# Kernel optimization log

Measured on AMD Instinct MI355X. Metric: run time of the kernel, lower is better.

The kernel has to match this reference:

```python
import jax, jax.numpy as jnp
import numpy as np

B, H, W, C = 16, 56, 56, 512
NUM_HEADS = 8
WS = 4  # window_size


def setup_inputs() -> dict:
    key = jax.random.key(0)
    k1, k2, k3, k4 = jax.random.split(key, 4)
    x = jax.random.normal(k1, (B, H, W, C), dtype=jnp.float32)
    w_qkv_h = jax.random.normal(k2, (3 * C, C), dtype=jnp.float32) * 0.02
    w_qkv_l = jax.random.normal(k3, (3 * C, C), dtype=jnp.float32) * 0.02
    w_proj = jax.random.normal(k4, (C, 2 * C), dtype=jnp.float32) * 0.02
    b_proj = jnp.zeros((C,), dtype=jnp.float32)
    return {"x": x, "w_qkv_h": w_qkv_h, "w_qkv_l": w_qkv_l,
            "w_proj": w_proj, "b_proj": b_proj}


def reference(x, w_qkv_h, w_qkv_l, w_proj, b_proj):
    b, h, w, c = x.shape
    nh = NUM_HEADS
    hd = c // nh
    nw = WS * WS  # tokens per window
    scale = c ** -0.5  # NOTE: original scales by full dim, not head dim

    # window partition: [B*H/ws*W/ws, ws*ws, C]
    xw = x.reshape(b, h // WS, WS, w // WS, WS, c)
    xw = xw.transpose(0, 1, 3, 2, 4, 5).reshape(-1, nw, c)

    # local branch qkv: [3, Nwin, nh, nw, hd]
    qkv_h = (xw @ w_qkv_h.T).reshape(-1, nw, 3, nh, hd).transpose(2, 0, 3, 1, 4)
    q_h, k_h, v_h = qkv_h[0], qkv_h[1], qkv_h[2]

    # global branch: average-pool each window to a single token [Nwin, 1, C]
    x_avg = x.reshape(b, h // WS, WS, w // WS, WS, c).mean(axis=(2, 4))
    x_avg = x_avg.reshape(-1, 1, c)
    qkv_l = (x_avg @ w_qkv_l.T).reshape(-1, 1, 3, nh, hd).transpose(2, 0, 3, 1, 4)
    q_l, k_l, v_l = qkv_l[0], qkv_l[1], qkv_l[2]

    # local window attention: [Nwin, nh, nw, nw]
    attn_h = jax.nn.softmax(jnp.einsum('bhqd,bhkd->bhqk', q_h, k_h) * scale, axis=-1)
    x_h = jnp.einsum('bhqk,bhkd->bhqd', attn_h, v_h)
    x_h = x_h.transpose(0, 2, 1, 3).reshape(-1, nw, c)

    # pooled global attention (1 token -> softmax over singleton = 1)
    attn_l = jax.nn.softmax(jnp.einsum('bhqd,bhkd->bhqk', q_l, k_l) * scale, axis=-1)
    x_l = jnp.einsum('bhqk,bhkd->bhqd', attn_l, v_l)
    x_l = x_l.transpose(0, 2, 1, 3).reshape(-1, 1, c)

    # concat local + broadcast global, project 2C -> C
    x_out = jnp.concatenate([x_h, jnp.broadcast_to(x_l, (x_l.shape[0], nw, c))], axis=-1)
    x_out = x_out @ w_proj.T + b_proj

    # window reverse
    x_out = x_out.reshape(b, h // WS, w // WS, WS, WS, c)
    x_out = x_out.transpose(0, 1, 3, 2, 4, 5).reshape(b, h, w, c)
    return x_out
```

## Files before the change

kernel.cpp:

```cpp
#include <hip/hip_runtime.h>


using bf16x8 = __attribute__((ext_vector_type(8))) short;
using f32x4  = __attribute__((ext_vector_type(4))) float;

#define SCALE 0.044194173824159216f

__device__ __forceinline__ unsigned short f2bf(float f) {
    union { float f; unsigned u; } v; v.f = f;
    unsigned u = v.u;
    return (unsigned short)((u + 0x7fffu + ((u >> 16) & 1u)) >> 16);
}

__device__ __forceinline__ void gl2lds16(const unsigned short* g, unsigned short* l) {
    __builtin_amdgcn_global_load_lds(
        (const __attribute__((address_space(1))) void*)g,
        (__attribute__((address_space(3))) void*)l, 16, 0, 0);
}

__global__ void k_prep_weights(const float* __restrict__ wqkv_h,
                               const float* __restrict__ wqkv_l,
                               const float* __restrict__ wproj,
                               unsigned short* __restrict__ WH,
                               unsigned short* __restrict__ WLV,
                               unsigned short* __restrict__ WP1,
                               unsigned short* __restrict__ WP2) {
    int i = blockIdx.x * 256 + threadIdx.x;
    if (i < 786432) {
        WH[i] = f2bf(wqkv_h[i]);
    } else {
        int j = i - 786432;
        int r = j >> 18;
        int t = j & 262143;
        int n = t >> 9, k = t & 511;
        if (r == 0)      WLV[t] = f2bf(wqkv_l[(1024 + n) * 512 + k]);
        else if (r == 1) WP1[t] = f2bf(wproj[n * 1024 + k]);
        else             WP2[t] = f2bf(wproj[n * 1024 + 512 + k]);
    }
}

__global__ void k_window_pool(const float* __restrict__ x,
                              unsigned short* __restrict__ XW,
                              unsigned short* __restrict__ XAVG) {
    int win = blockIdx.x * 2 + (threadIdx.x >> 7);
    int g = threadIdx.x & 127;
    int c = g * 4;
    int b = win / 196, rem = win % 196, wh = rem / 14, ww = rem % 14;
    float4 s = {0.f, 0.f, 0.f, 0.f};
    #pragma unroll
    for (int t = 0; t < 16; ++t) {
        int row = (b * 56 + wh * 4 + (t >> 2)) * 56 + ww * 4 + (t & 3);
        float4 v = *(const float4*)&x[(size_t)row * 512 + c];
        uint2 pk;
        pk.x = (unsigned)f2bf(v.x) | ((unsigned)f2bf(v.y) << 16);
        pk.y = (unsigned)f2bf(v.z) | ((unsigned)f2bf(v.w) << 16);
        *(uint2*)&XW[(size_t)(win * 16 + t) * 512 + c] = pk;
        s.x += v.x; s.y += v.y; s.z += v.z; s.w += v.w;
    }
    uint2 pa;
    pa.x = (unsigned)f2bf(s.x * 0.0625f) | ((unsigned)f2bf(s.y * 0.0625f) << 16);
    pa.y = (unsigned)f2bf(s.z * 0.0625f) | ((unsigned)f2bf(s.w * 0.0625f) << 16);
    *(uint2*)&XAVG[(size_t)win * 512 + c] = pa;
}

template <int NT>
__global__ void k_gemm512(const unsigned short* __restrict__ A,
                          const unsigned short* __restrict__ Bw,
                          unsigned short* __restrict__ outB,
                          float* __restrict__ outF,
                          const float* __restrict__ bias) {
    int wave = threadIdx.x >> 6, lane = threadIdx.x & 63;
    int quad = lane >> 4, l16 = lane & 15;
    int m0 = blockIdx.x * 64 + wave * 16;
    int n0 = blockIdx.y * (NT * 16);
    f32x4 acc[NT] = {};
    const unsigned short* arow = A + (size_t)(m0 + l16) * 512 + quad * 8;
    for (int kk = 0; kk < 16; ++kk) {
        bf16x8 a = *(const bf16x8*)(arow + kk * 32);
        #pragma unroll
        for (int nt = 0; nt < NT; ++nt) {
            bf16x8 b = *(const bf16x8*)(Bw + (size_t)(n0 + nt * 16 + l16) * 512 + kk * 32 + quad * 8);
            acc[nt] = __builtin_amdgcn_mfma_f32_16x16x32_bf16(a, b, acc[nt], 0, 0, 0);
        }
    }
    #pragma unroll
    for (int nt = 0; nt < NT; ++nt) {
        int col = n0 + nt * 16 + l16;
        float bv = (bias != nullptr) ? bias[col] : 0.f;
        #pragma unroll
        for (int r = 0; r < 4; ++r) {
            int row = m0 + quad * 4 + r;
            if (outF != nullptr) outF[(size_t)row * 512 + col] = acc[nt][r] + bv;
            else                 outB[(size_t)row * 512 + col] = f2bf(acc[nt][r]);
        }
    }
}

__global__ void __launch_bounds__(512, 4) k_fused(const unsigned short* __restrict__ XW,
                                                  const unsigned short* __restrict__ WH,
                                                  unsigned short* __restrict__ XH) {
    __shared__ __align__(16) char smem[81920];

    const int tid  = threadIdx.x;
    const int wave = tid >> 6, lane = tid & 63;
    const int quad = lane >> 4, l16 = lane & 15;
    const int mh = wave >> 2, nq = wave & 3;

    int id   = blockIdx.y * 392 + blockIdx.x;
    int s_   = id >> 3;
    int tb   = (id & 7) * 49 + (s_ >> 3);
    int head = s_ & 7;
    const int m0 = tb * 128;

    size_t aof[2];
    #pragma unroll
    for (int i = 0; i < 2; ++i) {
        int u = i * 512 + tid;
        int n = u >> 3;
        int gu = (u & 7) ^ (n & 7);
        aof[i] = (size_t)(m0 + n) * 512 + gu * 8;
    }
    size_t bof[3];
    #pragma unroll
    for (int i = 0; i < 3; ++i) {
        int u = i * 512 + tid;
        int n = u >> 3;
        int gu = (u & 7) ^ (n & 7);
        int nrow = (n >> 6) * 512 + head * 64 + (n & 63);
        bof[i] = (size_t)nrow * 512 + gu * 8;
    }

    unsigned short* const bufA[2] = { (unsigned short*)smem,
                                      (unsigned short*)(smem + 40960) };
    unsigned short* const bufB[2] = { (unsigned short*)(smem + 16384),
                                      (unsigned short*)(smem + 40960 + 16384) };

    f32x4 acc[4][3] = {};
    const int sx = l16 & 7;

    #pragma unroll
    for (int i = 0; i < 2; ++i)
        gl2lds16(XW + aof[i], bufA[0] + (i * 512 + wave * 64) * 8);
    #pragma unroll
    for (int i = 0; i < 3; ++i)
        gl2lds16(WH + bof[i], bufB[0] + (i * 512 + wave * 64) * 8);
    __syncthreads();

    #pragma unroll
    for (int ch = 0; ch < 8; ++ch) {
        unsigned short* As = bufA[ch & 1];
        unsigned short* Bs = bufB[ch & 1];
        if (ch < 7) {
            unsigned short* An = bufA[(ch + 1) & 1];
            unsigned short* Bn = bufB[(ch + 1) & 1];
            #pragma unroll
            for (int i = 0; i < 2; ++i)
                gl2lds16(XW + aof[i] + (ch + 1) * 64, An + (i * 512 + wave * 64) * 8);
            #pragma unroll
            for (int i = 0; i < 3; ++i)
                gl2lds16(WH + bof[i] + (ch + 1) * 64, Bn + (i * 512 + wave * 64) * 8);
        }
        #pragma unroll
        for (int kk = 0; kk < 2; ++kk) {
            int su = ((kk * 4 + quad) ^ sx) * 8;
            bf16x8 a[4], b[3];
            #pragma unroll
            for (int mf = 0; mf < 4; ++mf) {
                int row = mh * 64 + mf * 16 + l16;
                a[mf] = *(const bf16x8*)&As[row * 64 + (((kk * 4 + quad) ^ (row & 7)) ^ sx ^ (row & 7)) * 8];
            }
            #pragma unroll
            for (int j = 0; j < 3; ++j) {
                int brow = nq * 48 + j * 16 + l16;
                b[j] = *(const bf16x8*)&Bs[brow * 64 + (((kk * 4 + quad) ^ (brow & 7)) ^ sx ^ (brow & 7)) * 8];
            }
            #pragma unroll
            for (int mf = 0; mf < 4; ++mf)
                #pragma unroll
                for (int j = 0; j < 3; ++j)
                    acc[mf][j] = __builtin_amdgcn_mfma_f32_16x16x32_bf16(a[mf], b[j], acc[mf][j], 0, 0, 0);
        }
        __syncthreads();
    }

    {
        char* att = smem + mh * 33792;
        unsigned short* qs  = (unsigned short*)att;
        unsigned short* ks  = (unsigned short*)(att + 9216);
        unsigned short* vts = (unsigned short*)(att + 18432);
        #pragma unroll
        for (int j = 0; j < 3; ++j) {
            int cb = nq * 48 + j * 16;
            #pragma unroll
            for (int mf = 0; mf < 4; ++mf) {
                #pragma unroll
                for (int r = 0; r < 4; ++r) {
                    int tok = mf * 16 + quad * 4 + r;
                    unsigned short hv = f2bf(acc[mf][j][r]);
                    if (cb < 64)       qs[tok * 72 + cb + l16] = hv;
                    else if (cb < 128) ks[tok * 72 + (cb - 64) + l16] = hv;
                    else               vts[(cb - 128 + l16) * 88 + tok] = hv;
                }
            }
        }
    }
    __syncthreads();

    char* att = smem + (wave >> 2) * 33792;
    unsigned short* qs  = (unsigned short*)att;
    unsigned short* ks  = (unsigned short*)(att + 9216);
    unsigned short* vts = (unsigned short*)(att + 18432);
    unsigned short* Ps  = (unsigned short*)(att + 29696);
    const int lw = wave & 3, t0 = lw * 16;

    if (lw == 3) {
        #pragma unroll
        for (int i = 0; i < 16; ++i) vts[lane * 88 + 64 + i] = 0;
    }
    {
        int prow = lane >> 2, pc = 16 + (lane & 3) * 4;
        #pragma unroll
        for (int i = 0; i < 4; ++i) Ps[lw * 512 + prow * 32 + pc + i] = 0;
    }

    f32x4 sacc = {};
    {
        bf16x8 a0 = *(const bf16x8*)&qs[(t0 + l16) * 72 + quad * 8];
        bf16x8 b0 = *(const bf16x8*)&ks[(t0 + l16) * 72 + quad * 8];
        sacc = __builtin_amdgcn_mfma_f32_16x16x32_bf16(a0, b0, sacc, 0, 0, 0);
        bf16x8 a1 = *(const bf16x8*)&qs[(t0 + l16) * 72 + 32 + quad * 8];
        bf16x8 b1 = *(const bf16x8*)&ks[(t0 + l16) * 72 + 32 + quad * 8];
        sacc = __builtin_amdgcn_mfma_f32_16x16x32_bf16(a1, b1, sacc, 0, 0, 0);
    }
    float p[4];
    #pragma unroll
    for (int r = 0; r < 4; ++r) {
        float v = sacc[r] * SCALE;
        float m = v;
        m = fmaxf(m, __shfl_xor(m, 1));
        m = fmaxf(m, __shfl_xor(m, 2));
        m = fmaxf(m, __shfl_xor(m, 4));
        m = fmaxf(m, __shfl_xor(m, 8));
        float e = __expf(v - m);
        float sm = e;
        sm += __shfl_xor(sm, 1);
        sm += __shfl_xor(sm, 2);
        sm += __shfl_xor(sm, 4);
        sm += __shfl_xor(sm, 8);
        p[r] = e / sm;
    }
    #pragma unroll
    for (int r = 0; r < 4; ++r)
        Ps[lw * 512 + (quad * 4 + r) * 32 + l16] = f2bf(p[r]);

    bf16x8 pa = *(const bf16x8*)&Ps[lw * 512 + l16 * 32 + quad * 8];
    #pragma unroll
    for (int nt = 0; nt < 4; ++nt) {
        f32x4 y = {};
        bf16x8 bv = *(const bf16x8*)&vts[(nt * 16 + l16) * 88 + t0 + quad * 8];
        y = __builtin_amdgcn_mfma_f32_16x16x32_bf16(pa, bv, y, 0, 0, 0);
        #pragma unroll
        for (int r = 0; r < 4; ++r)
            XH[(size_t)(m0 + (wave >> 2) * 64 + t0 + quad * 4 + r) * 512 + head * 64 + nt * 16 + l16] = f2bf(y[r]);
    }
}

__global__ void __launch_bounds__(256, 2) k_gemm_proj(const unsigned short* __restrict__ XH,
                                                      const unsigned short* __restrict__ WP1,
                                                      const float* __restrict__ G,
                                                      float* __restrict__ out) {
    __shared__ __align__(16) char smem[65536];

    const int wave = threadIdx.x >> 6, lane = threadIdx.x & 63;
    const int quad = lane >> 4, l16 = lane & 15;

    int id = blockIdx.y * 392 + blockIdx.x;
    int s  = id >> 3;
    int xb = (id & 7) * 49 + (s >> 2);
    int yb = s & 3;
    const int m0 = xb * 128, n0 = yb * 128;
    const int wm = (wave >> 1) * 64;
    const int wn = (wave & 1) * 64;

    size_t aofs[4], bofs[4];
    #pragma unroll
    for (int i = 0; i < 4; ++i) {
        int u = (wave * 4 + i) * 64 + lane;
        int n = u >> 3;
        int gu = (lane & 7) ^ (n & 7);
        aofs[i] = (size_t)(m0 + n) * 512 + gu * 8;
        bofs[i] = (size_t)(n0 + n) * 512 + gu * 8;
    }

    unsigned short* const bufA[2] = { (unsigned short*)smem,
                                      (unsigned short*)(smem + 32768) };
    unsigned short* const bufB[2] = { (unsigned short*)(smem + 16384),
                                      (unsigned short*)(smem + 32768 + 16384) };

    f32x4 acc[4][4] = {};
    const int sx = l16 & 7;

    #pragma unroll
    for (int i = 0; i < 4; ++i) {
        gl2lds16(XH + aofs[i], bufA[0] + (wave * 4 + i) * 512);
        gl2lds16(WP1 + bofs[i], bufB[0] + (wave * 4 + i) * 512);
    }
    __syncthreads();

    #pragma unroll
    for (int ch = 0; ch < 8; ++ch) {
        unsigned short* As = bufA[ch & 1];
        unsigned short* Bs = bufB[ch & 1];
        if (ch < 7) {
            unsigned short* An = bufA[(ch + 1) & 1];
            unsigned short* Bn = bufB[(ch + 1) & 1];
            #pragma unroll
            for (int i = 0; i < 4; ++i) {
                gl2lds16(XH + aofs[i] + (ch + 1) * 64, An + (wave * 4 + i) * 512);
                gl2lds16(WP1 + bofs[i] + (ch + 1) * 64, Bn + (wave * 4 + i) * 512);
            }
        }
        #pragma unroll
        for (int kk = 0; kk < 2; ++kk) {
            int su = ((kk * 4 + quad) ^ sx) * 8;
            bf16x8 a[4], b[4];
            #pragma unroll
            for (int mf = 0; mf < 4; ++mf)
                a[mf] = *(const bf16x8*)&As[(wm + mf * 16 + l16) * 64 + su];
            #pragma unroll
            for (int j = 0; j < 4; ++j)
                b[j] = *(const bf16x8*)&Bs[(wn + j * 16 + l16) * 64 + su];
            #pragma unroll
            for (int mf = 0; mf < 4; ++mf)
                #pragma unroll
                for (int j = 0; j < 4; ++j)
                    acc[mf][j] = __builtin_amdgcn_mfma_f32_16x16x32_bf16(a[mf], b[j], acc[mf][j], 0, 0, 0);
        }
        __syncthreads();
    }

    #pragma unroll
    for (int mf = 0; mf < 4; ++mf) {
        #pragma unroll
        for (int r = 0; r < 4; ++r) {
            int tl  = wm + mf * 16 + quad * 4 + r;
            int gt  = m0 + tl;
            int win = gt >> 4, tw = gt & 15;
            int bb = win / 196, rem = win % 196;
            int wh = rem / 14, ww = rem % 14;
            int orow = (bb * 56 + wh * 4 + (tw >> 2)) * 56 + ww * 4 + (tw & 3);
            #pragma unroll
            for (int j = 0; j < 4; ++j) {
                int ncol = n0 + wn + j * 16 + l16;
                out[(size_t)orow * 512 + ncol] = acc[mf][j][r] + G[(size_t)win * 512 + ncol];
            }
        }
    }
}

extern "C" void kernel_launch(void* const* d_in, const int* in_sizes, int n_in,
                              void* d_out, int out_size, void* d_ws, size_t ws_size,
                              hipStream_t stream) {
    const float* x      = (const float*)d_in[0];
    const float* wqkv_h = (const float*)d_in[1];
    const float* wqkv_l = (const float*)d_in[2];
    const float* wproj  = (const float*)d_in[3];
    const float* bproj  = (const float*)d_in[4];
    float* out = (float*)d_out;

    char* ws = (char*)d_ws;
    unsigned short* WH   = (unsigned short*)(ws + 0);
    unsigned short* WLV  = (unsigned short*)(ws + 1572864);
    unsigned short* WP1  = (unsigned short*)(ws + 2097152);
    unsigned short* WP2  = (unsigned short*)(ws + 2621440);
    unsigned short* XW   = (unsigned short*)(ws + 3145728);
    unsigned short* XAVG = (unsigned short*)(ws + 54525952);
    unsigned short* VL   = (unsigned short*)(ws + 57737216);
    float*          G    = (float*)(ws + 60948480);
    unsigned short* XH   = (unsigned short*)(ws + 67371008);

    k_prep_weights<<<dim3(6144), dim3(256), 0, stream>>>(wqkv_h, wqkv_l, wproj, WH, WLV, WP1, WP2);
    k_window_pool<<<dim3(1568), dim3(256), 0, stream>>>(x, XW, XAVG);
    k_gemm512<2><<<dim3(49, 16), dim3(256), 0, stream>>>(XAVG, WLV, VL, (float*)nullptr, (const float*)nullptr);
    k_gemm512<2><<<dim3(49, 16), dim3(256), 0, stream>>>(VL, WP2, (unsigned short*)nullptr, G, bproj);
    k_fused<<<dim3(392, 8), dim3(512), 0, stream>>>(XW, WH, XH);
    k_gemm_proj<<<dim3(392, 4), dim3(256), 0, stream>>>(XH, WP1, G, out);
}
```

Before: 392.5 us.

## Load GEMM weight operands directly to registers, widen pooling stores, shrink LDS

The fused QKV+attention kernel now reads its weight (B) fragments straight from global memory into registers instead of staging them through LDS. It also swaps __syncthreads for explicit waitcnt plus barrier, cuts LDS from 80KB to 64KB and tightens the V-transpose padding, and remaps the block-to-tile order. The projection GEMM drops LDS staging entirely, loading both operands from global memory with unrolled K loops, and its occupancy hint rises to 4 blocks. The window-pool kernel handles 8 channels per thread with 16-byte stores. These changes aim to cut LDS traffic, barrier cost and LDS-limited occupancy, at the risk of more uncoalesced global and L2 reads.

```diff
diff --git a/kernel.cpp b/kernel.cpp
--- a/kernel.cpp
+++ b/kernel.cpp
@@ -10,6 +10,10 @@
     union { float f; unsigned u; } v; v.f = f;
     unsigned u = v.u;
     return (unsigned short)((u + 0x7fffu + ((u >> 16) & 1u)) >> 16);
+}
+
+__device__ __forceinline__ unsigned pk2(float a, float b) {
+    return (unsigned)f2bf(a) | ((unsigned)f2bf(b) << 16);
 }
 
 __device__ __forceinline__ void gl2lds16(const unsigned short* g, unsigned short* l) {
@@ -42,25 +46,30 @@
 __global__ void k_window_pool(const float* __restrict__ x,
                               unsigned short* __restrict__ XW,
                               unsigned short* __restrict__ XAVG) {
-    int win = blockIdx.x * 2 + (threadIdx.x >> 7);
-    int g = threadIdx.x & 127;
-    int c = g * 4;
+    int win = blockIdx.x * 4 + (threadIdx.x >> 6);
+    int g = threadIdx.x & 63;
+    int c = g * 8;
     int b = win / 196, rem = win % 196, wh = rem / 14, ww = rem % 14;
-    float4 s = {0.f, 0.f, 0.f, 0.f};
+    float s0 = 0.f, s1 = 0.f, s2 = 0.f, s3 = 0.f, s4 = 0.f, s5 = 0.f, s6 = 0.f, s7 = 0.f;
     #pragma unroll
     for (int t = 0; t < 16; ++t) {
         int row = (b * 56 + wh * 4 + (t >> 2)) * 56 + ww * 4 + (t & 3);
-        float4 v = *(const float4*)&x[(size_t)row * 512 + c];
-        uint2 pk;
-        pk.x = (unsigned)f2bf(v.x) | ((unsigned)f2bf(v.y) << 16);
-        pk.y = (unsigned)f2bf(v.z) | ((unsigned)f2bf(v.w) << 16);
-        *(uint2*)&XW[(size_t)(win * 16 + t) * 512 + c] = pk;
-        s.x += v.x; s.y += v.y; s.z += v.z; s.w += v.w;
-    }
-    uint2 pa;
-    pa.x = (unsigned)f2bf(s.x * 0.0625f) | ((unsigned)f2bf(s.y * 0.0625f) << 16);
-    pa.y = (unsigned)f2bf(s.z * 0.0625f) | ((unsigned)f2bf(s.w * 0.0625f) << 16);
-    *(uint2*)&XAVG[(size_t)win * 512 + c] = pa;
+        const float* p = &x[(size_t)row * 512 + c];
+        float4 v0 = *(const float4*)p;
+        float4 v1 = *(const float4*)(p + 4);
+        uint4 pk;
+        pk.x = pk2(v0.x, v0.y); pk.y = pk2(v0.z, v0.w);
+        pk.z = pk2(v1.x, v1.y); pk.w = pk2(v1.z, v1.w);
+        *(uint4*)&XW[(size_t)(win * 16 + t) * 512 + c] = pk;
+        s0 += v0.x; s1 += v0.y; s2 += v0.z; s3 += v0.w;
+        s4 += v1.x; s5 += v1.y; s6 += v1.z; s7 += v1.w;
+    }
+    uint4 pa;
+    pa.x = pk2(s0 * 0.0625f, s1 * 0.0625f);
+    pa.y = pk2(s2 * 0.0625f, s3 * 0.0625f);
+    pa.z = pk2(s4 * 0.0625f, s5 * 0.0625f);
+    pa.w = pk2(s6 * 0.0625f, s7 * 0.0625f);
+    *(uint4*)&XAVG[(size_t)win * 512 + c] = pa;
 }
 
 template <int NT>
@@ -99,7 +108,7 @@
 __global__ void __launch_bounds__(512, 4) k_fused(const unsigned short* __restrict__ XW,
                                                   const unsigned short* __restrict__ WH,
                                                   unsigned short* __restrict__ XH) {
-    __shared__ __align__(16) char smem[81920];
+    __shared__ __align__(16) char smem[65536];
 
     const int tid  = threadIdx.x;
     const int wave = tid >> 6, lane = tid & 63;
@@ -107,84 +116,73 @@
     const int mh = wave >> 2, nq = wave & 3;
 
     int id   = blockIdx.y * 392 + blockIdx.x;
-    int s_   = id >> 3;
-    int tb   = (id & 7) * 49 + (s_ >> 3);
-    int head = s_ & 7;
+    int w_   = (id & 7) * 392 + (id >> 3);
+    int tb   = w_ >> 3, head = w_ & 7;
     const int m0 = tb * 128;
 
-    size_t aof[2];
+    int aof[2];
     #pragma unroll
     for (int i = 0; i < 2; ++i) {
         int u = i * 512 + tid;
         int n = u >> 3;
         int gu = (u & 7) ^ (n & 7);
-        aof[i] = (size_t)(m0 + n) * 512 + gu * 8;
-    }
-    size_t bof[3];
-    #pragma unroll
-    for (int i = 0; i < 3; ++i) {
-        int u = i * 512 + tid;
-        int n = u >> 3;
-        int gu = (u & 7) ^ (n & 7);
-        int nrow = (n >> 6) * 512 + head * 64 + (n & 63);
-        bof[i] = (size_t)nrow * 512 + gu * 8;
+        aof[i] = (m0 + n) * 512 + gu * 8;
+    }
+    const unsigned short* bp[3];
+    #pragma unroll
+    for (int j = 0; j < 3; ++j) {
+        int cb = nq * 48 + j * 16;
+        int row = (cb >> 6) * 512 + head * 64 + (cb & 63) + l16;
+        bp[j] = WH + (size_t)row * 512 + quad * 8;
     }
 
     unsigned short* const bufA[2] = { (unsigned short*)smem,
-                                      (unsigned short*)(smem + 40960) };
-    unsigned short* const bufB[2] = { (unsigned short*)(smem + 16384),
-                                      (unsigned short*)(smem + 40960 + 16384) };
-
+                                      (unsigned short*)(smem + 16384) };
     f32x4 acc[4][3] = {};
     const int sx = l16 & 7;
 
     #pragma unroll
     for (int i = 0; i < 2; ++i)
         gl2lds16(XW + aof[i], bufA[0] + (i * 512 + wave * 64) * 8);
-    #pragma unroll
-    for (int i = 0; i < 3; ++i)
-        gl2lds16(WH + bof[i], bufB[0] + (i * 512 + wave * 64) * 8);
-    __syncthreads();
 
     #pragma unroll
     for (int ch = 0; ch < 8; ++ch) {
-        unsigned short* As = bufA[ch & 1];
-        unsigned short* Bs = bufB[ch & 1];
+        bf16x8 b[2][3];
+        #pragma unroll
+        for (int kk = 0; kk < 2; ++kk)
+            #pragma unroll
+            for (int j = 0; j < 3; ++j)
+                b[kk][j] = *(const bf16x8*)(bp[j] + ch * 64 + kk * 32);
         if (ch < 7) {
             unsigned short* An = bufA[(ch + 1) & 1];
-            unsigned short* Bn = bufB[(ch + 1) & 1];
             #pragma unroll
             for (int i = 0; i < 2; ++i)
                 gl2lds16(XW + aof[i] + (ch + 1) * 64, An + (i * 512 + wave * 64) * 8);
-            #pragma unroll
-            for (int i = 0; i < 3; ++i)
-                gl2lds16(WH + bof[i] + (ch + 1) * 64, Bn + (i * 512 + wave * 64) * 8);
-        }
+        }
+        if (ch < 7) asm volatile("s_waitcnt vmcnt(2)" ::: "memory");
+        else        asm volatile("s_waitcnt vmcnt(0)" ::: "memory");
+        __builtin_amdgcn_s_barrier();
+
+        unsigned short* As = bufA[ch & 1];
         #pragma unroll
         for (int kk = 0; kk < 2; ++kk) {
             int su = ((kk * 4 + quad) ^ sx) * 8;
-            bf16x8 a[4], b[3];
-            #pragma unroll
-            for (int mf = 0; mf < 4; ++mf) {
-                int row = mh * 64 + mf * 16 + l16;
-                a[mf] = *(const bf16x8*)&As[row * 64 + (((kk * 4 + quad) ^ (row & 7)) ^ sx ^ (row & 7)) * 8];
-            }
-            #pragma unroll
-            for (int j = 0; j < 3; ++j) {
-                int brow = nq * 48 + j * 16 + l16;
-                b[j] = *(const bf16x8*)&Bs[brow * 64 + (((kk * 4 + quad) ^ (brow & 7)) ^ sx ^ (brow & 7)) * 8];
-            }
+            bf16x8 a[4];
+            #pragma unroll
+            for (int mf = 0; mf < 4; ++mf)
+                a[mf] = *(const bf16x8*)&As[(mh * 64 + mf * 16 + l16) * 64 + su];
             #pragma unroll
             for (int mf = 0; mf < 4; ++mf)
                 #pragma unroll
                 for (int j = 0; j < 3; ++j)
-                    acc[mf][j] = __builtin_amdgcn_mfma_f32_16x16x32_bf16(a[mf], b[j], acc[mf][j], 0, 0, 0);
-        }
-        __syncthreads();
+                    acc[mf][j] = __builtin_amdgcn_mfma_f32_16x16x32_bf16(a[mf], b[kk][j], acc[mf][j], 0, 0, 0);
+        }
+        asm volatile("s_waitcnt lgkmcnt(0)" ::: "memory");
+        __builtin_amdgcn_s_barrier();
     }
 
     {
-        char* att = smem + mh * 33792;
+        char* att = smem + mh * 32768;
         unsigned short* qs  = (unsigned short*)att;
         unsigned short* ks  = (unsigned short*)(att + 9216);
         unsigned short* vts = (unsigned short*)(att + 18432);
@@ -199,28 +197,28 @@
                     unsigned short hv = f2bf(acc[mf][j][r]);
                     if (cb < 64)       qs[tok * 72 + cb + l16] = hv;
                     else if (cb < 128) ks[tok * 72 + (cb - 64) + l16] = hv;
-                    else               vts[(cb - 128 + l16) * 88 + tok] = hv;
+                    else               vts[(cb - 128 + l16) * 80 + tok] = hv;
                 }
             }
         }
     }
     __syncthreads();
 
-    char* att = smem + (wave >> 2) * 33792;
+    char* att = smem + mh * 32768;
     unsigned short* qs  = (unsigned short*)att;
     unsigned short* ks  = (unsigned short*)(att + 9216);
     unsigned short* vts = (unsigned short*)(att + 18432);
-    unsigned short* Ps  = (unsigned short*)(att + 29696);
-    const int lw = wave & 3, t0 = lw * 16;
-
-    if (lw == 3) {
-        #pragma unroll
-        for (int i = 0; i < 16; ++i) vts[lane * 88 + 64 + i] = 0;
+    unsigned short* Ps  = (unsigned short*)(att + 28672);
+    const int t0 = nq * 16;
+
+    if (nq == 3) {
+        #pragma unroll
+        for (int i = 0; i < 16; ++i) vts[lane * 80 + 64 + i] = 0;
     }
     {
         int prow = lane >> 2, pc = 16 + (lane & 3) * 4;
         #pragma unroll
-        for (int i = 0; i < 4; ++i) Ps[lw * 512 + prow * 32 + pc + i] = 0;
+        for (int i = 0; i < 4; ++i) Ps[nq * 512 + prow * 32 + pc + i] = 0;
     }
 
     f32x4 sacc = {};
@@ -251,26 +249,24 @@
     }
     #pragma unroll
     for (int r = 0; r < 4; ++r)
-        Ps[lw * 512 + (quad * 4 + r) * 32 + l16] = f2bf(p[r]);
-
-    bf16x8 pa = *(const bf16x8*)&Ps[lw * 512 + l16 * 32 + quad * 8];
+        Ps[nq * 512 + (quad * 4 + r) * 32 + l16] = f2bf(p[r]);
+
+    bf16x8 pa = *(const bf16x8*)&Ps[nq * 512 + l16 * 32 + quad * 8];
     #pragma unroll
     for (int nt = 0; nt < 4; ++nt) {
         f32x4 y = {};
-        bf16x8 bv = *(const bf16x8*)&vts[(nt * 16 + l16) * 88 + t0 + quad * 8];
+        bf16x8 bv = *(const bf16x8*)&vts[(nt * 16 + l16) * 80 + t0 + quad * 8];
         y = __builtin_amdgcn_mfma_f32_16x16x32_bf16(pa, bv, y, 0, 0, 0);
         #pragma unroll
         for (int r = 0; r < 4; ++r)
-            XH[(size_t)(m0 + (wave >> 2) * 64 + t0 + quad * 4 + r) * 512 + head * 64 + nt * 16 + l16] = f2bf(y[r]);
-    }
-}
-
-__global__ void __launch_bounds__(256, 2) k_gemm_proj(const unsigned short* __restrict__ XH,
+            XH[(size_t)(m0 + mh * 64 + t0 + quad * 4 + r) * 512 + head * 64 + nt * 16 + l16] = f2bf(y[r]);
+    }
+}
+
+__global__ void __launch_bounds__(256, 4) k_gemm_proj(const unsigned short* __restrict__ XH,
                                                       const unsigned short* __restrict__ WP1,
                                                       const float* __restrict__ G,
                                                       float* __restrict__ out) {
-    __shared__ __align__(16) char smem[65536];
-
     const int wave = threadIdx.x >> 6, lane = threadIdx.x & 63;
     const int quad = lane >> 4, l16 = lane & 15;
 
@@ -282,61 +278,28 @@
     const int wm = (wave >> 1) * 64;
     const int wn = (wave & 1) * 64;
 
-    size_t aofs[4], bofs[4];
+    const unsigned short* ap[4];
+    const unsigned short* bp[4];
     #pragma unroll
     for (int i = 0; i < 4; ++i) {
-        int u = (wave * 4 + i) * 64 + lane;
-        int n = u >> 3;
-        int gu = (lane & 7) ^ (n & 7);
-        aofs[i] = (size_t)(m0 + n) * 512 + gu * 8;
-        bofs[i] = (size_t)(n0 + n) * 512 + gu * 8;
-    }
-
-    unsigned short* const bufA[2] = { (unsigned short*)smem,
-                                      (unsigned short*)(smem + 32768) };
-    unsigned short* const bufB[2] = { (unsigned short*)(smem + 16384),
-                                      (unsigned short*)(smem + 32768 + 16384) };
+        ap[i] = XH  + (size_t)(m0 + wm + i * 16 + l16) * 512 + quad * 8;
+        bp[i] = WP1 + (size_t)(n0 + wn + i * 16 + l16) * 512 + quad * 8;
+    }
 
     f32x4 acc[4][4] = {};
-    const int sx = l16 & 7;
-
-    #pragma unroll
-    for (int i = 0; i < 4; ++i) {
-        gl2lds16(XH + aofs[i], bufA[0] + (wave * 4 + i) * 512);
-        gl2lds16(WP1 + bofs[i], bufB[0] + (wave * 4 + i) * 512);
-    }
-    __syncthreads();
-
-    #pragma unroll
-    for (int ch = 0; ch < 8; ++ch) {
-        unsigned short* As = bufA[ch & 1];
-        unsigned short* Bs = bufB[ch & 1];
-        if (ch < 7) {
-            unsigned short* An = bufA[(ch + 1) & 1];
-            unsigned short* Bn = bufB[(ch + 1) & 1];
-            #pragma unroll
-            for (int i = 0; i < 4; ++i) {
-                gl2lds16(XH + aofs[i] + (ch + 1) * 64, An + (wave * 4 + i) * 512);
-                gl2lds16(WP1 + bofs[i] + (ch + 1) * 64, Bn + (wave * 4 + i) * 512);
-            }
-        }
-        #pragma unroll
-        for (int kk = 0; kk < 2; ++kk) {
-            int su = ((kk * 4 + quad) ^ sx) * 8;
-            bf16x8 a[4], b[4];
-            #pragma unroll
-            for (int mf = 0; mf < 4; ++mf)
-                a[mf] = *(const bf16x8*)&As[(wm + mf * 16 + l16) * 64 + su];
+
+    #pragma unroll 4
+    for (int kk = 0; kk < 16; ++kk) {
+        bf16x8 a[4], b[4];
+        #pragma unroll
+        for (int mf = 0; mf < 4; ++mf) a[mf] = *(const bf16x8*)(ap[mf] + kk * 32);
+        #pragma unroll
+        for (int j = 0; j < 4; ++j)    b[j]  = *(const bf16x8*)(bp[j] + kk * 32);
+        #pragma unroll
+        for (int mf = 0; mf < 4; ++mf)
             #pragma unroll
             for (int j = 0; j < 4; ++j)
-                b[j] = *(const bf16x8*)&Bs[(wn + j * 16 + l16) * 64 + su];
-            #pragma unroll
-            for (int mf = 0; mf < 4; ++mf)
-                #pragma unroll
-                for (int j = 0; j < 4; ++j)
-                    acc[mf][j] = __builtin_amdgcn_mfma_f32_16x16x32_bf16(a[mf], b[j], acc[mf][j], 0, 0, 0);
-        }
-        __syncthreads();
+                acc[mf][j] = __builtin_amdgcn_mfma_f32_16x16x32_bf16(a[mf], b[j], acc[mf][j], 0, 0, 0);
     }
 
     #pragma unroll
@@ -380,7 +343,7 @@
     unsigned short* XH   = (unsigned short*)(ws + 67371008);
 
     k_prep_weights<<<dim3(6144), dim3(256), 0, stream>>>(wqkv_h, wqkv_l, wproj, WH, WLV, WP1, WP2);
-    k_window_pool<<<dim3(1568), dim3(256), 0, stream>>>(x, XW, XAVG);
+    k_window_pool<<<dim3(784), dim3(256), 0, stream>>>(x, XW, XAVG);
     k_gemm512<2><<<dim3(49, 16), dim3(256), 0, stream>>>(XAVG, WLV, VL, (float*)nullptr, (const float*)nullptr);
     k_gemm512<2><<<dim3(49, 16), dim3(256), 0, stream>>>(VL, WP2, (unsigned short*)nullptr, G, bproj);
     k_fused<<<dim3(392, 8), dim3(512), 0, stream>>>(XW, WH, XH);
```

Measured after the change: 525.2 us. +33.8%, slower.
